# Performance work log

Hardware: AMD Instinct MI355X
Metric: run time of the kernel (lower is better)

Reference implementation:

```python
import jax, jax.numpy as jnp
import numpy as np

N = 1_000_000   # total nodes
D = 128         # hidden_dim
B = 1024        # number of graphs (segments)
E = 2_000_000   # edges (unused by forward math, kept for signature fidelity)
EPS = 1e-16     # PyG softmax denominator epsilon


def setup_inputs() -> dict:
    key = jax.random.key(0)
    k1, k2, k3, k4 = jax.random.split(key, 4)
    x = jax.random.normal(k1, (N, D), dtype=jnp.float32)
    edge_index = jax.random.randint(k2, (2, E), 0, N, dtype=jnp.int32)
    batch = jnp.sort(jax.random.randint(k3, (N,), 0, B, dtype=jnp.int32))
    # Linear(hidden_dim, 1) parameters
    W = jax.random.normal(k4, (1, D), dtype=jnp.float32) * (1.0 / np.sqrt(D))
    b = jnp.zeros((1,), dtype=jnp.float32)
    return {"x": x, "edge_index": edge_index, "batch": batch, "W": W, "b": b}


def reference(x, edge_index, batch, W, b):
    # scores = Linear(x).squeeze(-1)  -> [N]
    scores = (x @ W.T + b)[:, 0]
    # pyg_softmax: segment-wise numerically-stable softmax over `batch`
    seg_max = jax.ops.segment_max(scores, batch, num_segments=B)          # [B]
    ex = jnp.exp(scores - seg_max[batch])                                  # [N]
    seg_sum = jax.ops.segment_sum(ex, batch, num_segments=B)              # [B]
    attn = ex / (seg_sum[batch] + EPS)                                     # [N]
    # global_add_pool of attention-weighted features -> [B, D]
    gx = jax.ops.segment_sum(x * attn[:, None], batch, num_segments=B)
    return gx
```

## Files before the change

### kernel.cpp

```cpp
#include <hip/hip_runtime.h>
#include <math.h>


#define DIM 128
#define NEG_HUGE (-3.0e38f)

__global__ void seg_offsets_kernel(const int* __restrict__ batch,
                                   int* __restrict__ off, int N, int B) {
    int i = blockIdx.x * blockDim.x + threadIdx.x;
    if (i >= N) return;
    int bi = batch[i];
    int bp = (i == 0) ? -1 : batch[i - 1];
    for (int s = bp + 1; s <= bi; ++s) off[s] = i;
    if (i == N - 1) {
        for (int s = bi + 1; s <= B; ++s) off[s] = N;
    }
}

__global__ __launch_bounds__(256) void gap_online_kernel(
    const float* __restrict__ x,
    const int*   __restrict__ off,
    const float* __restrict__ W,
    const float* __restrict__ bias,
    float*       __restrict__ out)
{
    const int seg  = blockIdx.x;
    const int tid  = threadIdx.x;
    const int wave = tid >> 6;
    const int lane = tid & 63;
    const int half = lane >> 5;
    const int hl   = lane & 31;

    const int start = off[seg];
    const int end   = off[seg + 1];

    const float4 wv = ((const float4*)W)[hl];
    const float  b0 = bias[0];

    float  m = NEG_HUGE;
    float  l = 0.0f;
    float4 acc = make_float4(0.f, 0.f, 0.f, 0.f);

    int p = start + wave * 8;

    float4 xv[4];
    #pragma unroll
    for (int k = 0; k < 4; ++k) {
        int row = p + 2 * k + half;
        xv[k] = (row < end) ? ((const float4*)(x + (size_t)row * DIM))[hl]
                            : make_float4(0.f, 0.f, 0.f, 0.f);
    }

    for (; p < end; p += 32) {
        float4 xn[4];
        #pragma unroll
        for (int k = 0; k < 4; ++k) {
            int row = p + 32 + 2 * k + half;
            xn[k] = (row < end) ? ((const float4*)(x + (size_t)row * DIM))[hl]
                                : make_float4(0.f, 0.f, 0.f, 0.f);
        }

        float s[4];
        #pragma unroll
        for (int k = 0; k < 4; ++k)
            s[k] = xv[k].x * wv.x + xv[k].y * wv.y + xv[k].z * wv.z + xv[k].w * wv.w;

        #pragma unroll
        for (int offd = 16; offd > 0; offd >>= 1) {
            #pragma unroll
            for (int k = 0; k < 4; ++k)
                s[k] += __shfl_xor(s[k], offd, 64);
        }

        #pragma unroll
        for (int k = 0; k < 4; ++k) {
            int  row   = p + 2 * k + half;
            bool valid = row < end;
            float sk    = valid ? (s[k] + b0) : NEG_HUGE;
            float m_new = fmaxf(m, sk);
            float alpha = __expf(m - m_new);
            float w     = valid ? __expf(sk - m_new) : 0.0f;
            l     = l * alpha + w;
            acc.x = acc.x * alpha + w * xv[k].x;
            acc.y = acc.y * alpha + w * xv[k].y;
            acc.z = acc.z * alpha + w * xv[k].z;
            acc.w = acc.w * alpha + w * xv[k].w;
            m     = m_new;
            xv[k] = xn[k];
        }
    }

    __shared__ float sm[8];
    __shared__ float sl[8];
    __shared__ float sacc[8][DIM];

    const int sid = wave * 2 + half;
    sacc[sid][4 * hl + 0] = acc.x;
    sacc[sid][4 * hl + 1] = acc.y;
    sacc[sid][4 * hl + 2] = acc.z;
    sacc[sid][4 * hl + 3] = acc.w;
    if (hl == 0) { sm[sid] = m; sl[sid] = l; }
    __syncthreads();

    if (tid < DIM) {
        float m_tot = NEG_HUGE;
        #pragma unroll
        for (int h = 0; h < 8; ++h) m_tot = fmaxf(m_tot, sm[h]);
        float num = 0.0f, den = 0.0f;
        #pragma unroll
        for (int h = 0; h < 8; ++h) {
            float a = __expf(sm[h] - m_tot);
            num += sacc[h][tid] * a;
            den += sl[h] * a;
        }
        out[(size_t)seg * DIM + tid] = num / (den + 1e-16f);
    }
}

extern "C" void kernel_launch(void* const* d_in, const int* in_sizes, int n_in,
                              void* d_out, int out_size, void* d_ws, size_t ws_size,
                              hipStream_t stream) {
    const float* x     = (const float*)d_in[0];
    const int*   batch = (const int*)d_in[2];
    const float* W     = (const float*)d_in[3];
    const float* bias  = (const float*)d_in[4];
    float*       out   = (float*)d_out;

    const int N = in_sizes[2];
    const int B = out_size / DIM;

    int* off = (int*)d_ws;

    seg_offsets_kernel<<<(N + 255) / 256, 256, 0, stream>>>(batch, off, N, B);
    gap_online_kernel<<<B, 256, 0, stream>>>(x, off, W, bias, out);
}
```

Baseline: 667.1 us.

## Split each segment across multiple blocks and merge softmax partials in second kernel

Each graph segment is now divided into eight chunks processed by separate blocks, so the grid has B*8 blocks instead of B. This raises occupancy and memory-level parallelism on a bandwidth-bound 512MB streaming pass. Each block writes its partial max, sum and weighted accumulator to workspace, and a new merge kernel combines them. The inner online-softmax update is also batched per 4-row tile to cut the number of exp rescales, at the cost of an extra launch and workspace traffic.

```diff
diff --git a/kernel.cpp b/kernel.cpp
--- a/kernel.cpp
+++ b/kernel.cpp
@@ -3,6 +3,7 @@
 
 
 #define DIM 128
+#define CHUNKS 8
 #define NEG_HUGE (-3.0e38f)
 
 __global__ void seg_offsets_kernel(const int* __restrict__ batch,
@@ -17,22 +18,27 @@
     }
 }
 
-__global__ __launch_bounds__(256) void gap_online_kernel(
+__global__ __launch_bounds__(256) void gap_partial_kernel(
     const float* __restrict__ x,
     const int*   __restrict__ off,
     const float* __restrict__ W,
     const float* __restrict__ bias,
-    float*       __restrict__ out)
+    float*       __restrict__ ws_acc,
+    float*       __restrict__ ws_ml)
 {
-    const int seg  = blockIdx.x;
-    const int tid  = threadIdx.x;
-    const int wave = tid >> 6;
-    const int lane = tid & 63;
-    const int half = lane >> 5;
-    const int hl   = lane & 31;
+    const int seg   = blockIdx.x / CHUNKS;
+    const int chunk = blockIdx.x % CHUNKS;
+    const int tid   = threadIdx.x;
+    const int wave  = tid >> 6;
+    const int lane  = tid & 63;
+    const int half  = lane >> 5;
+    const int hl    = lane & 31;
 
-    const int start = off[seg];
-    const int end   = off[seg + 1];
+    const int sstart = off[seg];
+    const int send   = off[seg + 1];
+    const int len    = send - sstart;
+    const int cs     = sstart + (int)(((long long)len * chunk) / CHUNKS);
+    const int ce     = sstart + (int)(((long long)len * (chunk + 1)) / CHUNKS);
 
     const float4 wv = ((const float4*)W)[hl];
     const float  b0 = bias[0];
@@ -41,23 +47,23 @@
     float  l = 0.0f;
     float4 acc = make_float4(0.f, 0.f, 0.f, 0.f);
 
-    int p = start + wave * 8;
+    int p = cs + wave * 8;
 
     float4 xv[4];
     #pragma unroll
     for (int k = 0; k < 4; ++k) {
         int row = p + 2 * k + half;
-        xv[k] = (row < end) ? ((const float4*)(x + (size_t)row * DIM))[hl]
-                            : make_float4(0.f, 0.f, 0.f, 0.f);
+        xv[k] = (row < ce) ? ((const float4*)(x + (size_t)row * DIM))[hl]
+                           : make_float4(0.f, 0.f, 0.f, 0.f);
     }
 
-    for (; p < end; p += 32) {
+    for (; p < ce; p += 32) {
         float4 xn[4];
         #pragma unroll
         for (int k = 0; k < 4; ++k) {
             int row = p + 32 + 2 * k + half;
-            xn[k] = (row < end) ? ((const float4*)(x + (size_t)row * DIM))[hl]
-                                : make_float4(0.f, 0.f, 0.f, 0.f);
+            xn[k] = (row < ce) ? ((const float4*)(x + (size_t)row * DIM))[hl]
+                               : make_float4(0.f, 0.f, 0.f, 0.f);
         }
 
         float s[4];
@@ -72,22 +78,29 @@
                 s[k] += __shfl_xor(s[k], offd, 64);
         }
 
+        bool valid[4];
         #pragma unroll
         for (int k = 0; k < 4; ++k) {
-            int  row   = p + 2 * k + half;
-            bool valid = row < end;
-            float sk    = valid ? (s[k] + b0) : NEG_HUGE;
-            float m_new = fmaxf(m, sk);
-            float alpha = __expf(m - m_new);
-            float w     = valid ? __expf(sk - m_new) : 0.0f;
-            l     = l * alpha + w;
-            acc.x = acc.x * alpha + w * xv[k].x;
-            acc.y = acc.y * alpha + w * xv[k].y;
-            acc.z = acc.z * alpha + w * xv[k].z;
-            acc.w = acc.w * alpha + w * xv[k].w;
-            m     = m_new;
-            xv[k] = xn[k];
+            valid[k] = (p + 2 * k + half) < ce;
+            s[k] = valid[k] ? (s[k] + b0) : NEG_HUGE;
         }
+        const float tile_m = fmaxf(fmaxf(s[0], s[1]), fmaxf(s[2], s[3]));
+        const float m_new  = fmaxf(m, tile_m);
+        const float alpha  = __expf(m - m_new);
+        float w[4];
+        #pragma unroll
+        for (int k = 0; k < 4; ++k)
+            w[k] = valid[k] ? __expf(s[k] - m_new) : 0.0f;
+
+        l = l * alpha + ((w[0] + w[1]) + (w[2] + w[3]));
+        acc.x = acc.x * alpha + ((w[0]*xv[0].x + w[1]*xv[1].x) + (w[2]*xv[2].x + w[3]*xv[3].x));
+        acc.y = acc.y * alpha + ((w[0]*xv[0].y + w[1]*xv[1].y) + (w[2]*xv[2].y + w[3]*xv[3].y));
+        acc.z = acc.z * alpha + ((w[0]*xv[0].z + w[1]*xv[1].z) + (w[2]*xv[2].z + w[3]*xv[3].z));
+        acc.w = acc.w * alpha + ((w[0]*xv[0].w + w[1]*xv[1].w) + (w[2]*xv[2].w + w[3]*xv[3].w));
+        m = m_new;
+
+        #pragma unroll
+        for (int k = 0; k < 4; ++k) xv[k] = xn[k];
     }
 
     __shared__ float sm[8];
@@ -103,18 +116,48 @@
     __syncthreads();
 
     if (tid < DIM) {
-        float m_tot = NEG_HUGE;
+        float m_p = NEG_HUGE;
         #pragma unroll
-        for (int h = 0; h < 8; ++h) m_tot = fmaxf(m_tot, sm[h]);
+        for (int h = 0; h < 8; ++h) m_p = fmaxf(m_p, sm[h]);
         float num = 0.0f, den = 0.0f;
         #pragma unroll
         for (int h = 0; h < 8; ++h) {
-            float a = __expf(sm[h] - m_tot);
+            float a = __expf(sm[h] - m_p);
             num += sacc[h][tid] * a;
             den += sl[h] * a;
         }
-        out[(size_t)seg * DIM + tid] = num / (den + 1e-16f);
+        ws_acc[(size_t)blockIdx.x * DIM + tid] = num;
+        if (tid == 0) {
+            ws_ml[(size_t)blockIdx.x * 2 + 0] = m_p;
+            ws_ml[(size_t)blockIdx.x * 2 + 1] = den;
+        }
     }
+}
+
+__global__ __launch_bounds__(DIM) void gap_merge_kernel(
+    const float* __restrict__ ws_acc,
+    const float* __restrict__ ws_ml,
+    float*       __restrict__ out)
+{
+    const int seg = blockIdx.x;
+    const int t   = threadIdx.x;
+
+    float mc[CHUNKS], lc[CHUNKS];
+    float m_tot = NEG_HUGE;
+    #pragma unroll
+    for (int c = 0; c < CHUNKS; ++c) {
+        mc[c] = ws_ml[(size_t)(seg * CHUNKS + c) * 2 + 0];
+        lc[c] = ws_ml[(size_t)(seg * CHUNKS + c) * 2 + 1];
+        m_tot = fmaxf(m_tot, mc[c]);
+    }
+    float num = 0.0f, den = 0.0f;
+    #pragma unroll
+    for (int c = 0; c < CHUNKS; ++c) {
+        float a = __expf(mc[c] - m_tot);
+        num += ws_acc[(size_t)(seg * CHUNKS + c) * DIM + t] * a;
+        den += lc[c] * a;
+    }
+    out[(size_t)seg * DIM + t] = num / (den + 1e-16f);
 }
 
 extern "C" void kernel_launch(void* const* d_in, const int* in_sizes, int n_in,
@@ -129,8 +172,11 @@
     const int N = in_sizes[2];
     const int B = out_size / DIM;
 
-    int* off = (int*)d_ws;
+    float* ws_acc = (float*)d_ws;
+    float* ws_ml  = ws_acc + (size_t)B * CHUNKS * DIM;
+    int*   off    = (int*)(ws_ml + (size_t)B * CHUNKS * 2);
 
     seg_offsets_kernel<<<(N + 255) / 256, 256, 0, stream>>>(batch, off, N, B);
-    gap_online_kernel<<<B, 256, 0, stream>>>(x, off, W, bias, out);
+    gap_partial_kernel<<<B * CHUNKS, 256, 0, stream>>>(x, off, W, bias, ws_acc, ws_ml);
+    gap_merge_kernel<<<B, DIM, 0, stream>>>(ws_acc, ws_ml, out);
 }
```

Measured after the change: 669.2 us. No clear change (+0.3%).
